# Kernel tuning notes

Measured on AMD Instinct MI355X. Metric: run time of the kernel, lower is better.

## Reference

```python
import jax, jax.numpy as jnp
import numpy as np

N_ELEM = 5
N_ROWS = 16            # height slices contained in the minibatch
N = 512                # sample_size_n
MB = N_ROWS * N        # minibatch_size = 8192
NVOX = MB * N          # n_voxel_minibatch
N_LINES = 12
LINE_GROUPS = [3, 2, 3, 2, 2]
SAMPLE_SIZE_CM = np.float32(0.01)
PROBE_CTS = np.float32(1.0e5)
FL_RATIO = np.float32(0.0017)   # fl_sig_collecting_ratio
SA_ADJ = np.float32(1.0)        # solid_angle_adjustment_factor
SA_THETA = np.float32(1.0)      # selfAb == False -> SA_theta = 1


def _rotate(arr, theta):
    # torch affine_grid + grid_sample(bilinear, padding_mode='border', align_corners=False)
    # arr: (E, C, H, W); rotation matrix rows [cos, -sin, 0], [sin, cos, 0]
    E, C, H, W = arr.shape
    cos, sin = jnp.cos(theta), jnp.sin(theta)
    xs = (2.0 * jnp.arange(W, dtype=arr.dtype) + 1.0) / W - 1.0
    ys = (2.0 * jnp.arange(H, dtype=arr.dtype) + 1.0) / H - 1.0
    gy, gx = jnp.meshgrid(ys, xs, indexing='ij')      # (H, W)
    x_in = cos * gx - sin * gy
    y_in = sin * gx + cos * gy
    ix = jnp.clip(((x_in + 1.0) * W - 1.0) * 0.5, 0.0, W - 1.0)  # border padding
    iy = jnp.clip(((y_in + 1.0) * H - 1.0) * 0.5, 0.0, H - 1.0)
    x0 = jnp.floor(ix); y0 = jnp.floor(iy)
    wx = ix - x0; wy = iy - y0
    x0i = x0.astype(jnp.int32); y0i = y0.astype(jnp.int32)
    x1i = jnp.minimum(x0i + 1, W - 1); y1i = jnp.minimum(y0i + 1, H - 1)
    g = lambda yi, xi: arr[:, :, yi, xi]              # -> (E, C, H, W)
    return (g(y0i, x0i) * (1 - wx) * (1 - wy) + g(y0i, x1i) * wx * (1 - wy)
            + g(y1i, x0i) * (1 - wx) * wy + g(y1i, x1i) * wx * wy)


def setup_inputs() -> dict:
    key = jax.random.key(0)
    k1, k2, k3 = jax.random.split(key, 3)
    xp = jax.random.uniform(k1, (N_ELEM, N_ROWS, N, N), dtype=jnp.float32)
    probe_attCS_ls = jax.random.uniform(k2, (N_ELEM,), dtype=jnp.float32) * 10.0
    detected_fl_unit_concentration = jax.random.uniform(k3, (N_LINES,), dtype=jnp.float32)
    line_element_idx = jnp.asarray(np.repeat(np.arange(N_ELEM), LINE_GROUPS).astype(np.int32))
    theta = jnp.float32(np.pi / 6)
    return {"xp": xp, "probe_attCS_ls": probe_attCS_ls,
            "detected_fl_unit_concentration": detected_fl_unit_concentration,
            "theta": theta, "line_element_idx": line_element_idx}


def reference(xp, probe_attCS_ls, detected_fl_unit_concentration, theta, line_element_idx):
    # rotate concentration grid and flatten beam rows: (E, MB, N)
    conc = _rotate(xp, theta).reshape(N_ELEM, MB, N)
    # Beer-Lambert attenuation: per-element lac summed over elements, cumsum along beam
    lac = jnp.einsum('e,ebs->bs', probe_attCS_ls, conc)                       # (MB, N)
    att_acc = jnp.pad(jnp.cumsum(lac, axis=1) * (SAMPLE_SIZE_CM / N),
                      ((0, 0), (1, 0)))                                       # (MB, N+1)
    attenuation_flat = jnp.exp(-att_acc[:, :-1]).reshape(NVOX)
    transmission = att_acc[:, -1]                                             # (MB,)
    # fluorescence map: each line picks its element's concentration
    conc_flat = conc.reshape(N_ELEM, NVOX)
    fl_map = conc_flat[line_element_idx] * detected_fl_unit_concentration[:, None]  # (L, NVOX)
    probe_after = PROBE_CTS * attenuation_flat
    fl_sig = (probe_after[None, :] * fl_map * SA_THETA).reshape(N_LINES, MB, N).sum(axis=-1)
    fl_sig = fl_sig * FL_RATIO * SA_ADJ                                       # (L, MB)
    return fl_sig, transmission
```

## Files before the change

kernel.cpp:

```cpp
#include <hip/hip_runtime.h>
#include <hip/hip_bf16.h>

#define N_ELEM   5
#define NW       512
#define MB_ROWS  8192
#define N_LINES  12
#define SCALE    (0.01f / 512.0f)
#define FL_CONST 170.0f

__global__ __launch_bounds__(512) void fused_fl_kernel(
    const float* __restrict__ xp,
    const float* __restrict__ attCS,
    const float* __restrict__ dfl,
    const float* __restrict__ theta_p,
    const int*   __restrict__ lidx,
    float*       __restrict__ out)
{
    const int bid = blockIdx.x;
    const int t   = bid >> 3;
    const int c   = (bid & 7) + 8 * (t >> 6);
    const int g   = t & 63;
    const int irow0 = g << 3;

    const int tid  = threadIdx.x;
    const int r    = tid & 7;
    const int sc   = tid >> 3;
    const int lane = tid & 63;
    const int w    = tid >> 6;

    const float theta = theta_p[0];
    const float cs = cosf(theta);
    const float sn = sinf(theta);

    const int irow = irow0 + r;
    const float gy = (2.0f * (float)irow + 1.0f) * (1.0f / 512.0f) - 1.0f;

    const size_t plane_c = (size_t)c * (512 * 512);
    const size_t estride = (size_t)16 * 512 * 512;
    const float* base = xp + plane_c;

    const float a0 = attCS[0], a1 = attCS[1], a2 = attCS[2], a3 = attCS[3], a4 = attCS[4];

    __shared__ float s_lac[2][8][72];
    __shared__ float s_att[2][8][72];
    __shared__ float s_part[8][8][5];
    __shared__ float s_S[8][5];

    float se0 = 0.f, se1 = 0.f, se2 = 0.f, se3 = 0.f, se4 = 0.f;
    float carry = 0.f;

    for (int k = 0; k < 8; ++k) {
        const int kb = k & 1;
        const int s = sc + (k << 6);

        const float gx = (2.0f * (float)s + 1.0f) * (1.0f / 512.0f) - 1.0f;
        const float x_in = cs * gx - sn * gy;
        const float y_in = sn * gx + cs * gy;
        float ix = ((x_in + 1.0f) * 512.0f - 1.0f) * 0.5f;
        float iy = ((y_in + 1.0f) * 512.0f - 1.0f) * 0.5f;
        ix = fminf(fmaxf(ix, 0.0f), 511.0f);
        iy = fminf(fmaxf(iy, 0.0f), 511.0f);

        const float x0f = floorf(ix);
        const float y0f = floorf(iy);
        const float wx = ix - x0f;
        const float wy = iy - y0f;
        const int x0 = (int)x0f;
        const int y0 = (int)y0f;
        const int x1 = min(x0 + 1, 511);
        const int y1 = min(y0 + 1, 511);

        const float w00 = (1.0f - wx) * (1.0f - wy);
        const float w01 = wx * (1.0f - wy);
        const float w10 = (1.0f - wx) * wy;
        const float w11 = wx * wy;

        const int o00 = y0 * 512 + x0;
        const int o01 = y0 * 512 + x1;
        const int o10 = y1 * 512 + x0;
        const int o11 = y1 * 512 + x1;

        float c0, c1, c2, c3, c4;
        {
            const float* p = base;
            c0 = w00 * p[o00] + w01 * p[o01] + w10 * p[o10] + w11 * p[o11];
            p += estride;
            c1 = w00 * p[o00] + w01 * p[o01] + w10 * p[o10] + w11 * p[o11];
            p += estride;
            c2 = w00 * p[o00] + w01 * p[o01] + w10 * p[o10] + w11 * p[o11];
            p += estride;
            c3 = w00 * p[o00] + w01 * p[o01] + w10 * p[o10] + w11 * p[o11];
            p += estride;
            c4 = w00 * p[o00] + w01 * p[o01] + w10 * p[o10] + w11 * p[o11];
        }
        float lac = a0 * c0;
        lac = fmaf(a1, c1, lac);
        lac = fmaf(a2, c2, lac);
        lac = fmaf(a3, c3, lac);
        lac = fmaf(a4, c4, lac);

        s_lac[kb][r][sc] = lac;
        __syncthreads();

        const float lv = s_lac[kb][w][lane];
        float v = lv;
#pragma unroll
        for (int off = 1; off < 64; off <<= 1) {
            float n = __shfl_up(v, off, 64);
            if (lane >= off) v += n;
        }
        const float tot = __shfl(v, 63, 64);
        const float excl = carry + v - lv;
        s_att[kb][w][lane] = __expf(-excl * SCALE);
        carry += tot;
        __syncthreads();

        const float att = s_att[kb][r][sc];
        se0 = fmaf(att, c0, se0);
        se1 = fmaf(att, c1, se1);
        se2 = fmaf(att, c2, se2);
        se3 = fmaf(att, c3, se3);
        se4 = fmaf(att, c4, se4);
    }

    if (lane == 0) {
        out[(size_t)N_LINES * MB_ROWS + (size_t)c * 512 + irow0 + w] = carry * SCALE;
    }

#pragma unroll
    for (int off = 32; off >= 8; off >>= 1) {
        se0 += __shfl_down(se0, off, 64);
        se1 += __shfl_down(se1, off, 64);
        se2 += __shfl_down(se2, off, 64);
        se3 += __shfl_down(se3, off, 64);
        se4 += __shfl_down(se4, off, 64);
    }
    if (lane < 8) {
        s_part[w][lane][0] = se0;
        s_part[w][lane][1] = se1;
        s_part[w][lane][2] = se2;
        s_part[w][lane][3] = se3;
        s_part[w][lane][4] = se4;
    }
    __syncthreads();

    if (tid < 40) {
        const int rr = tid & 7;
        const int e  = tid >> 3;
        float S = 0.f;
#pragma unroll
        for (int ww = 0; ww < 8; ++ww) S += s_part[ww][rr][e];
        s_S[rr][e] = S;
    }
    __syncthreads();

    if (tid < 96) {
        const int rr = tid / 12;
        const int l  = tid % 12;
        const size_t b = (size_t)c * 512 + irow0 + rr;
        out[(size_t)l * MB_ROWS + b] = FL_CONST * dfl[l] * s_S[rr][lidx[l]];
    }
}

extern "C" void kernel_launch(void* const* d_in, const int* in_sizes, int n_in,
                              void* d_out, int out_size, void* d_ws, size_t ws_size,
                              hipStream_t stream) {
    const float* xp    = (const float*)d_in[0];
    const float* attCS = (const float*)d_in[1];
    const float* dfl   = (const float*)d_in[2];
    const float* theta = (const float*)d_in[3];
    const int*   lidx  = (const int*)d_in[4];
    float* out = (float*)d_out;

    fused_fl_kernel<<<MB_ROWS / 8, 512, 0, stream>>>(xp, attCS, dfl, theta, lidx, out);
}
```

Before: 182.3 us.

## Stage rotated bounding-box tiles in LDS and map one wave per row

```diff
diff --git a/kernel.cpp b/kernel.cpp
--- a/kernel.cpp
+++ b/kernel.cpp
@@ -1,14 +1,13 @@
 #include <hip/hip_runtime.h>
 #include <hip/hip_bf16.h>
 
-#define N_ELEM   5
-#define NW       512
 #define MB_ROWS  8192
 #define N_LINES  12
 #define SCALE    (0.01f / 512.0f)
 #define FL_CONST 170.0f
-
-__global__ __launch_bounds__(512) void fused_fl_kernel(
+#define TAREA    3072
+
+__global__ __launch_bounds__(512, 4) void fused_fl_kernel(
     const float* __restrict__ xp,
     const float* __restrict__ attCS,
     const float* __restrict__ dfl,
@@ -23,8 +22,6 @@
     const int irow0 = g << 3;
 
     const int tid  = threadIdx.x;
-    const int r    = tid & 7;
-    const int sc   = tid >> 3;
     const int lane = tid & 63;
     const int w    = tid >> 6;
 
@@ -32,27 +29,68 @@
     const float cs = cosf(theta);
     const float sn = sinf(theta);
 
-    const int irow = irow0 + r;
-    const float gy = (2.0f * (float)irow + 1.0f) * (1.0f / 512.0f) - 1.0f;
-
-    const size_t plane_c = (size_t)c * (512 * 512);
+    const int irow = irow0 + w;
+    const float gy  = (2.0f * (float)irow + 1.0f) * (1.0f / 512.0f) - 1.0f;
+    const float gya = (2.0f * (float)irow0       + 1.0f) * (1.0f / 512.0f) - 1.0f;
+    const float gyb = (2.0f * (float)(irow0 + 7) + 1.0f) * (1.0f / 512.0f) - 1.0f;
+
     const size_t estride = (size_t)16 * 512 * 512;
-    const float* base = xp + plane_c;
+    const float* base = xp + (size_t)c * (512 * 512);
 
     const float a0 = attCS[0], a1 = attCS[1], a2 = attCS[2], a3 = attCS[3], a4 = attCS[4];
 
-    __shared__ float s_lac[2][8][72];
-    __shared__ float s_att[2][8][72];
-    __shared__ float s_part[8][8][5];
-    __shared__ float s_S[8][5];
+    __shared__ float s_tile[5 * TAREA];
 
     float se0 = 0.f, se1 = 0.f, se2 = 0.f, se3 = 0.f, se4 = 0.f;
     float carry = 0.f;
 
     for (int k = 0; k < 8; ++k) {
-        const int kb = k & 1;
-        const int s = sc + (k << 6);
-
+        const float gxa = (2.0f * (float)(k << 6)        + 1.0f) * (1.0f / 512.0f) - 1.0f;
+        const float gxb = (2.0f * (float)((k << 6) + 63) + 1.0f) * (1.0f / 512.0f) - 1.0f;
+
+        const float xi00 = cs * gxa - sn * gya, xi01 = cs * gxa - sn * gyb;
+        const float xi10 = cs * gxb - sn * gya, xi11 = cs * gxb - sn * gyb;
+        const float yi00 = sn * gxa + cs * gya, yi01 = sn * gxa + cs * gyb;
+        const float yi10 = sn * gxb + cs * gya, yi11 = sn * gxb + cs * gyb;
+
+        float xmn = fminf(fminf(xi00, xi01), fminf(xi10, xi11));
+        float xmx = fmaxf(fmaxf(xi00, xi01), fmaxf(xi10, xi11));
+        float ymn = fminf(fminf(yi00, yi01), fminf(yi10, yi11));
+        float ymx = fmaxf(fmaxf(yi00, yi01), fmaxf(yi10, yi11));
+
+        float ixmn = fminf(fmaxf(((xmn + 1.0f) * 512.0f - 1.0f) * 0.5f, 0.0f), 511.0f);
+        float ixmx = fminf(fmaxf(((xmx + 1.0f) * 512.0f - 1.0f) * 0.5f, 0.0f), 511.0f);
+        float iymn = fminf(fmaxf(((ymn + 1.0f) * 512.0f - 1.0f) * 0.5f, 0.0f), 511.0f);
+        float iymx = fminf(fmaxf(((ymx + 1.0f) * 512.0f - 1.0f) * 0.5f, 0.0f), 511.0f);
+
+        const int bbx0 = (int)floorf(ixmn);
+        const int bbx1 = min((int)floorf(ixmx) + 2, 511);
+        const int bby0 = (int)floorf(iymn);
+        const int bby1 = min((int)floorf(iymx) + 2, 511);
+        const int W = bbx1 - bbx0 + 1;
+        int H = bby1 - bby0 + 1;
+
+        const int fast = (W <= 64 && H <= 48);
+        const int Wp = fast ? 64 : W;
+        int maxH = fast ? 48 : (TAREA / Wp);
+        if (H > maxH) H = maxH;
+
+        __syncthreads();
+
+#pragma unroll
+        for (int e = 0; e < 5; ++e) {
+            const float* plane = base + (size_t)e * estride;
+            float* tile = &s_tile[e * TAREA];
+            for (int yy = w; yy < H; yy += 8) {
+                const float* src = plane + (bby0 + yy) * 512 + bbx0;
+                float* dst = tile + yy * Wp;
+                if (lane < W) dst[lane] = src[lane];
+                if (64 + lane < W) dst[64 + lane] = src[64 + lane];
+            }
+        }
+        __syncthreads();
+
+        const int s = (k << 6) + lane;
         const float gx = (2.0f * (float)s + 1.0f) * (1.0f / 512.0f) - 1.0f;
         const float x_in = cs * gx - sn * gy;
         const float y_in = sn * gx + cs * gy;
@@ -75,90 +113,77 @@
         const float w10 = (1.0f - wx) * wy;
         const float w11 = wx * wy;
 
-        const int o00 = y0 * 512 + x0;
-        const int o01 = y0 * 512 + x1;
-        const int o10 = y1 * 512 + x0;
-        const int o11 = y1 * 512 + x1;
-
-        float c0, c1, c2, c3, c4;
+        const int ly0 = (y0 - bby0) * Wp;
+        const int ly1 = (y1 - bby0) * Wp;
+        const int lx0 = x0 - bbx0;
+        const int lx1 = x1 - bbx0;
+        const int o00 = ly0 + lx0, o01 = ly0 + lx1;
+        const int o10 = ly1 + lx0, o11 = ly1 + lx1;
+
+        float cv0, cv1, cv2, cv3, cv4;
         {
-            const float* p = base;
-            c0 = w00 * p[o00] + w01 * p[o01] + w10 * p[o10] + w11 * p[o11];
-            p += estride;
-            c1 = w00 * p[o00] + w01 * p[o01] + w10 * p[o10] + w11 * p[o11];
-            p += estride;
-            c2 = w00 * p[o00] + w01 * p[o01] + w10 * p[o10] + w11 * p[o11];
-            p += estride;
-            c3 = w00 * p[o00] + w01 * p[o01] + w10 * p[o10] + w11 * p[o11];
-            p += estride;
-            c4 = w00 * p[o00] + w01 * p[o01] + w10 * p[o10] + w11 * p[o11];
+            const float* tp = s_tile;
+            cv0 = w00 * tp[o00] + w01 * tp[o01] + w10 * tp[o10] + w11 * tp[o11];
+            tp += TAREA;
+            cv1 = w00 * tp[o00] + w01 * tp[o01] + w10 * tp[o10] + w11 * tp[o11];
+            tp += TAREA;
+            cv2 = w00 * tp[o00] + w01 * tp[o01] + w10 * tp[o10] + w11 * tp[o11];
+            tp += TAREA;
+            cv3 = w00 * tp[o00] + w01 * tp[o01] + w10 * tp[o10] + w11 * tp[o11];
+            tp += TAREA;
+            cv4 = w00 * tp[o00] + w01 * tp[o01] + w10 * tp[o10] + w11 * tp[o11];
         }
-        float lac = a0 * c0;
-        lac = fmaf(a1, c1, lac);
-        lac = fmaf(a2, c2, lac);
-        lac = fmaf(a3, c3, lac);
-        lac = fmaf(a4, c4, lac);
-
-        s_lac[kb][r][sc] = lac;
-        __syncthreads();
-
-        const float lv = s_lac[kb][w][lane];
-        float v = lv;
+
+        float lac = a0 * cv0;
+        lac = fmaf(a1, cv1, lac);
+        lac = fmaf(a2, cv2, lac);
+        lac = fmaf(a3, cv3, lac);
+        lac = fmaf(a4, cv4, lac);
+
+        float v = lac;
 #pragma unroll
         for (int off = 1; off < 64; off <<= 1) {
             float n = __shfl_up(v, off, 64);
             if (lane >= off) v += n;
         }
-        const float tot = __shfl(v, 63, 64);
-        const float excl = carry + v - lv;
-        s_att[kb][w][lane] = __expf(-excl * SCALE);
+        const float tot  = __shfl(v, 63, 64);
+        const float excl = carry + v - lac;
+        const float att  = __expf(-excl * SCALE);
         carry += tot;
-        __syncthreads();
-
-        const float att = s_att[kb][r][sc];
-        se0 = fmaf(att, c0, se0);
-        se1 = fmaf(att, c1, se1);
-        se2 = fmaf(att, c2, se2);
-        se3 = fmaf(att, c3, se3);
-        se4 = fmaf(att, c4, se4);
-    }
-
-    if (lane == 0) {
-        out[(size_t)N_LINES * MB_ROWS + (size_t)c * 512 + irow0 + w] = carry * SCALE;
+
+        se0 = fmaf(att, cv0, se0);
+        se1 = fmaf(att, cv1, se1);
+        se2 = fmaf(att, cv2, se2);
+        se3 = fmaf(att, cv3, se3);
+        se4 = fmaf(att, cv4, se4);
     }
 
 #pragma unroll
-    for (int off = 32; off >= 8; off >>= 1) {
+    for (int off = 32; off > 0; off >>= 1) {
         se0 += __shfl_down(se0, off, 64);
         se1 += __shfl_down(se1, off, 64);
         se2 += __shfl_down(se2, off, 64);
         se3 += __shfl_down(se3, off, 64);
         se4 += __shfl_down(se4, off, 64);
     }
-    if (lane < 8) {
-        s_part[w][lane][0] = se0;
-        s_part[w][lane][1] = se1;
-        s_part[w][lane][2] = se2;
-        s_part[w][lane][3] = se3;
-        s_part[w][lane][4] = se4;
-    }
-    __syncthreads();
-
-    if (tid < 40) {
-        const int rr = tid & 7;
-        const int e  = tid >> 3;
-        float S = 0.f;
-#pragma unroll
-        for (int ww = 0; ww < 8; ++ww) S += s_part[ww][rr][e];
-        s_S[rr][e] = S;
-    }
-    __syncthreads();
-
-    if (tid < 96) {
-        const int rr = tid / 12;
-        const int l  = tid % 12;
-        const size_t b = (size_t)c * 512 + irow0 + rr;
-        out[(size_t)l * MB_ROWS + b] = FL_CONST * dfl[l] * s_S[rr][lidx[l]];
+    const float S0 = __shfl(se0, 0, 64);
+    const float S1 = __shfl(se1, 0, 64);
+    const float S2 = __shfl(se2, 0, 64);
+    const float S3 = __shfl(se3, 0, 64);
+    const float S4 = __shfl(se4, 0, 64);
+
+    const size_t b = (size_t)c * 512 + irow;
+    if (lane == 0) {
+        out[(size_t)N_LINES * MB_ROWS + b] = carry * SCALE;
+    }
+    if (lane < N_LINES) {
+        const int li = lidx[lane];
+        float Ssel = S0;
+        Ssel = (li == 1) ? S1 : Ssel;
+        Ssel = (li == 2) ? S2 : Ssel;
+        Ssel = (li == 3) ? S3 : Ssel;
+        Ssel = (li == 4) ? S4 : Ssel;
+        out[(size_t)lane * MB_ROWS + b] = FL_CONST * dfl[lane] * Ssel;
     }
 }
 
```

After: 305.9 us. 67.8% more time.
